# Performance work log

Hardware: AMD Instinct MI355X
Metric: run time of the kernel (lower is better)

Reference implementation:

```python
import jax, jax.numpy as jnp
import numpy as np

N_NODES = 100000
N_EDGES = 3200000  # avg degree 32
IN_FEATS = 512
N_HIDDEN = 128
N_CLASSES = 64
K = 10  # n_layers of gated APPNP propagation


def setup_inputs() -> dict:
    key = jax.random.key(0)
    ks = jax.random.split(key, 6)
    features = jax.random.normal(ks[0], (N_NODES, IN_FEATS), dtype=jnp.float32)
    W1 = jax.random.normal(ks[1], (IN_FEATS, N_HIDDEN), dtype=jnp.float32) * (1.0 / np.sqrt(IN_FEATS))
    b1 = jnp.zeros((N_HIDDEN,), jnp.float32)
    W2 = jax.random.normal(ks[2], (N_HIDDEN, N_CLASSES), dtype=jnp.float32) * (1.0 / np.sqrt(N_HIDDEN))
    b2 = jnp.zeros((N_CLASSES,), jnp.float32)
    init_weight_y = jax.random.normal(ks[3], (IN_FEATS, N_CLASSES), dtype=jnp.float32) * (1.0 / np.sqrt(IN_FEATS))
    edge_index = jax.random.randint(ks[4], (2, N_EDGES), 0, N_NODES, dtype=jnp.int32)
    return {
        "features": features, "W1": W1, "b1": b1, "W2": W2, "b2": b2,
        "init_weight_y": init_weight_y, "edge_index": edge_index,
    }


def reference(features, W1, b1, W2, b2, init_weight_y, edge_index):
    # Eval-mode forward: feat/edge dropout are identity.
    src, dst = edge_index[0], edge_index[1]
    n = features.shape[0]
    # Symmetric GCN normalization D^{-1/2} A D^{-1/2} from in-degrees.
    deg = jax.ops.segment_sum(jnp.ones(src.shape, features.dtype), dst, num_segments=n)
    norm = jax.lax.rsqrt(jnp.clip(deg, 1.0))
    ew = (norm[src] * norm[dst])[:, None]  # [E,1] edge weights

    def spmm(x):  # A_hat @ x via gather-multiply-scatter
        return jax.ops.segment_sum(x[src] * ew, dst, num_segments=n)

    # feature transform: dropout(identity) -> linear -> relu
    h = jax.nn.relu(features @ W1 + b1)                      # [N,H]
    logits = jax.nn.softmax(features @ init_weight_y, axis=1)  # [N,C]
    # project predictions before propagation (APPNP propagates class scores)
    h0 = h @ W2 + b2                                         # [N,C]

    def step(carry, _):
        hc, lg = carry
        agg_lg = spmm(lg)                                    # neighbor soft labels
        # gate: per-node agreement between own and aggregated soft labels
        z = jax.nn.sigmoid(jnp.sum(lg * agg_lg, axis=1, keepdims=True))  # [N,1]
        h_new = z * spmm(hc) + (1.0 - z) * h0                # gated APPNP hop
        return (h_new, agg_lg), None

    (h_out, _), _ = jax.lax.scan(step, (h0, logits), None, length=K)
    return h_out
```

## Files before the change

kernel.cpp:

```cpp
#include <hip/hip_runtime.h>

typedef __attribute__((ext_vector_type(8))) short bf16x8;
typedef __attribute__((ext_vector_type(4))) short bf16x4;
typedef __attribute__((ext_vector_type(4))) float f32x4;
typedef __attribute__((ext_vector_type(4))) unsigned int u32x4;

__device__ __forceinline__ unsigned short f2bf(float f) {
  unsigned int u = __float_as_uint(f);
  u += 0x7fffu + ((u >> 16) & 1u);
  return (unsigned short)(u >> 16);
}
__device__ __forceinline__ float bflo(unsigned int w) { return __uint_as_float(w << 16); }
__device__ __forceinline__ float bfhi(unsigned int w) { return __uint_as_float(w & 0xffff0000u); }

__device__ __forceinline__ short* ldsp(short* base, int row, int rowbytes, int colshort) {
  int off = row * rowbytes + colshort * 2;
  off ^= ((row & 7) << 4);
  return (short*)((char*)base + off);
}

#define CHUNK 8192
#define NBMAX 512

__global__ __launch_bounds__(256) void k_bhist(const int* __restrict__ ei, int E, int NB,
                                               int* __restrict__ gcnt, int* __restrict__ wghist) {
  __shared__ int h[NBMAX];
  for (int t = threadIdx.x; t < NB; t += 256) h[t] = 0;
  __syncthreads();
  int base = blockIdx.x * CHUNK;
#pragma unroll
  for (int i = 0; i < CHUNK / 256; ++i) {
    int e = base + i * 256 + threadIdx.x;
    if (e < E) atomicAdd(&h[ei[E + e] >> 8], 1);
  }
  __syncthreads();
  for (int t = threadIdx.x; t < NB; t += 256) {
    int c = h[t];
    wghist[blockIdx.x * NBMAX + t] = c;
    if (c) atomicAdd(&gcnt[t], c);
  }
}

__global__ void k_bscan(const int* __restrict__ gcnt, int* __restrict__ bbase,
                        int* __restrict__ gcur, int* __restrict__ offs, int NB, int N) {
  __shared__ int sm[512];
  int t = threadIdx.x;
  int v = (t < NB) ? gcnt[t] : 0;
  sm[t] = v;
  __syncthreads();
  for (int o = 1; o < 512; o <<= 1) {
    int x = (t >= o) ? sm[t - o] : 0;
    __syncthreads();
    sm[t] += x;
    __syncthreads();
  }
  if (t < NB) { int e = sm[t] - v; bbase[t] = e; gcur[t] = e; }
  if (t == 511) { bbase[NB] = sm[511]; offs[N] = sm[511]; }
}

__global__ __launch_bounds__(256) void k_bucket(const int* __restrict__ ei,
                                                const int* __restrict__ wghist,
                                                int* __restrict__ gcur,
                                                int2* __restrict__ bpairs, int E, int NB) {
  __shared__ int lbase[NBMAX];
  __shared__ int lcur[NBMAX];
  for (int t = threadIdx.x; t < NB; t += 256) {
    int c = wghist[blockIdx.x * NBMAX + t];
    lbase[t] = c ? atomicAdd(&gcur[t], c) : 0;
    lcur[t] = 0;
  }
  __syncthreads();
  int base = blockIdx.x * CHUNK;
#pragma unroll
  for (int i = 0; i < CHUNK / 256; ++i) {
    int e = base + i * 256 + threadIdx.x;
    if (e < E) {
      int s = ei[e], d = ei[E + e];
      int b = d >> 8;
      int p = lbase[b] + atomicAdd(&lcur[b], 1);
      bpairs[p] = make_int2(s, d);
    }
  }
}

__global__ __launch_bounds__(256) void k_csr(const int2* __restrict__ bpairs,
                                             const int* __restrict__ bbase,
                                             int* __restrict__ offs, float* __restrict__ nrm,
                                             int* __restrict__ csr_src, int N) {
  __shared__ int hist[256];
  __shared__ int scan[256];
  __shared__ int cur[256];
  const int t = threadIdx.x;
  const int b = blockIdx.x;
  const int d0 = b << 8;
  const int nn = min(256, N - d0);
  const int base = bbase[b], end = bbase[b + 1];
  hist[t] = 0;
  __syncthreads();
  for (int e = base + t; e < end; e += 256) atomicAdd(&hist[bpairs[e].y - d0], 1);
  __syncthreads();
  int myc = hist[t];
  scan[t] = myc;
  __syncthreads();
  for (int o = 1; o < 256; o <<= 1) {
    int x = (t >= o) ? scan[t - o] : 0;
    __syncthreads();
    scan[t] += x;
    __syncthreads();
  }
  int excl = scan[t] - myc;
  if (t < nn) {
    offs[d0 + t] = base + excl;
    nrm[d0 + t] = rsqrtf(fmaxf((float)myc, 1.f));
  }
  cur[t] = excl;
  __syncthreads();
  for (int e = base + t; e < end; e += 256) {
    int2 pr = bpairs[e];
    int pos = atomicAdd(&cur[pr.y - d0], 1);
    csr_src[base + pos] = pr.x;
  }
}

__global__ void k_wprep(const float* __restrict__ W1, const float* __restrict__ Wy,
                        unsigned short* __restrict__ Wt) {
  int k = blockIdx.x, j = threadIdx.x;
  float v = (j < 128) ? W1[k * 128 + j] : Wy[k * 64 + (j - 128)];
  Wt[j * 512 + k] = f2bf(v);
}
__global__ void k_wprep2(const float* __restrict__ W2, unsigned short* __restrict__ Wt2) {
  int k = blockIdx.x, j = threadIdx.x;
  Wt2[j * 128 + k] = f2bf(W2[k * 64 + j]);
}

__global__ __launch_bounds__(256) void k_transform(
    const unsigned short* __restrict__ Wt, const unsigned short* __restrict__ Wt2,
    const float* __restrict__ X, const float* __restrict__ b1, const float* __restrict__ b2,
    const float* __restrict__ nrm,
    unsigned int* __restrict__ pk0, unsigned short* __restrict__ h0b, int n)
{
  __shared__ short Xs[128 * 32];
  __shared__ short Ws[192 * 32];
  __shared__ short Hs[128 * 128];
  __shared__ short W2s[64 * 128];

  const int tid = threadIdx.x;
  const int w = tid >> 6;
  const int lane = tid & 63;
  const int c = lane & 15;
  const int g = lane >> 4;
  const int m0 = blockIdx.x * 128;

#pragma unroll
  for (int i = 0; i < 4; ++i) {
    int cc = tid + i * 256;
    int j2 = cc >> 4, k8 = (cc & 15) * 8;
    bf16x8 v = *(const bf16x8*)&Wt2[j2 * 128 + k8];
    *(bf16x8*)ldsp(W2s, j2, 256, k8) = v;
  }

  f32x4 zero4 = {0.f, 0.f, 0.f, 0.f};
  f32x4 acc[2][12];
#pragma unroll
  for (int mi = 0; mi < 2; ++mi)
#pragma unroll
    for (int i = 0; i < 12; ++i) acc[mi][i] = zero4;

  const int xr = tid >> 1;
  const int xc = (tid & 1) * 16;
  const int xrow = m0 + xr;

  for (int kk = 0; kk < 512; kk += 32) {
    float4 f[4];
    if (xrow < n) {
      const float4* p = (const float4*)(X + (size_t)xrow * 512 + kk + xc);
      f[0] = p[0]; f[1] = p[1]; f[2] = p[2]; f[3] = p[3];
    } else {
      float4 z = {0.f, 0.f, 0.f, 0.f};
      f[0] = z; f[1] = z; f[2] = z; f[3] = z;
    }
    bf16x8 lo, hi;
    {
      const float* fp = (const float*)f;
#pragma unroll
      for (int q = 0; q < 8; ++q) { lo[q] = (short)f2bf(fp[q]); hi[q] = (short)f2bf(fp[8 + q]); }
    }
    *(bf16x8*)ldsp(Xs, xr, 64, xc) = lo;
    *(bf16x8*)ldsp(Xs, xr, 64, xc + 8) = hi;
#pragma unroll
    for (int i = 0; i < 3; ++i) {
      int cc = tid + i * 256;
      int j = cc >> 2, k8 = (cc & 3) * 8;
      bf16x8 v = *(const bf16x8*)&Wt[j * 512 + kk + k8];
      *(bf16x8*)ldsp(Ws, j, 64, k8) = v;
    }
    __syncthreads();
    bf16x8 bx0 = *(const bf16x8*)ldsp(Xs, w * 32 + c, 64, g * 8);
    bf16x8 bx1 = *(const bf16x8*)ldsp(Xs, w * 32 + 16 + c, 64, g * 8);
#pragma unroll
    for (int jt = 0; jt < 12; ++jt) {
      bf16x8 aw = *(const bf16x8*)ldsp(Ws, jt * 16 + c, 64, g * 8);
      acc[0][jt] = __builtin_amdgcn_mfma_f32_16x16x32_bf16(aw, bx0, acc[0][jt], 0, 0, 0);
      acc[1][jt] = __builtin_amdgcn_mfma_f32_16x16x32_bf16(aw, bx1, acc[1][jt], 0, 0, 0);
    }
    __syncthreads();
  }

  float lv[2][16];
  float inv_[2];
#pragma unroll
  for (int mi = 0; mi < 2; ++mi) {
    int m = w * 32 + mi * 16 + c;
#pragma unroll
    for (int jt = 0; jt < 8; ++jt) {
      int jb = jt * 16 + g * 4;
      bf16x4 hv;
#pragma unroll
      for (int q = 0; q < 4; ++q) {
        float hvf = fmaxf(acc[mi][jt][q] + b1[jb + q], 0.f);
        hv[q] = (short)f2bf(hvf);
      }
      *(bf16x4*)ldsp(Hs, m, 256, jb) = hv;
    }
    float mx = -3.4e38f;
#pragma unroll
    for (int t = 0; t < 4; ++t)
#pragma unroll
      for (int q = 0; q < 4; ++q) {
        float vv = acc[mi][8 + t][q];
        lv[mi][t * 4 + q] = vv;
        mx = fmaxf(mx, vv);
      }
    mx = fmaxf(mx, __shfl_xor(mx, 16, 64));
    mx = fmaxf(mx, __shfl_xor(mx, 32, 64));
    float sum = 0.f;
#pragma unroll
    for (int i = 0; i < 16; ++i) { lv[mi][i] = __expf(lv[mi][i] - mx); sum += lv[mi][i]; }
    sum += __shfl_xor(sum, 16, 64);
    sum += __shfl_xor(sum, 32, 64);
    inv_[mi] = 1.f / sum;
  }
  __syncthreads();

  f32x4 acc2[2][4];
#pragma unroll
  for (int mi = 0; mi < 2; ++mi)
#pragma unroll
    for (int i = 0; i < 4; ++i) acc2[mi][i] = zero4;
#pragma unroll
  for (int kk2 = 0; kk2 < 4; ++kk2) {
    bf16x8 bh0 = *(const bf16x8*)ldsp(Hs, w * 32 + c, 256, kk2 * 32 + g * 8);
    bf16x8 bh1 = *(const bf16x8*)ldsp(Hs, w * 32 + 16 + c, 256, kk2 * 32 + g * 8);
#pragma unroll
    for (int j2t = 0; j2t < 4; ++j2t) {
      bf16x8 a2 = *(const bf16x8*)ldsp(W2s, j2t * 16 + c, 256, kk2 * 32 + g * 8);
      acc2[0][j2t] = __builtin_amdgcn_mfma_f32_16x16x32_bf16(a2, bh0, acc2[0][j2t], 0, 0, 0);
      acc2[1][j2t] = __builtin_amdgcn_mfma_f32_16x16x32_bf16(a2, bh1, acc2[1][j2t], 0, 0, 0);
    }
  }

#pragma unroll
  for (int mi = 0; mi < 2; ++mi) {
    int m = w * 32 + mi * 16 + c;
    int grow = m0 + m;
    if (grow < n) {
      float nd = nrm[grow];
#pragma unroll
      for (int t = 0; t < 4; ++t) {
        int cb = t * 16 + g * 4;
        u32x4 pkv;
        bf16x4 hb;
#pragma unroll
        for (int q = 0; q < 4; ++q) {
          float lg  = lv[mi][t * 4 + q] * inv_[mi];
          float h0v = acc2[mi][t][q] + b2[cb + q];
          hb[q]  = (short)f2bf(h0v);
          pkv[q] = ((unsigned)f2bf(nd * h0v) << 16) | (unsigned)f2bf(nd * lg);
        }
        *(u32x4*)(pk0 + (size_t)grow * 64 + cb) = pkv;
        *(bf16x4*)(h0b + (size_t)grow * 64 + cb) = hb;
      }
    }
  }
}

__global__ __launch_bounds__(256) void k_prop(
    const int* __restrict__ offs, const int* __restrict__ csr_src,
    const unsigned int* __restrict__ pk_in, unsigned int* __restrict__ pk_out,
    const unsigned short* __restrict__ h0b, const float* __restrict__ nrm,
    float* __restrict__ final_out, int n, int last)
{
  const int lane = threadIdx.x & 63;
  const int node = blockIdx.x * 4 + (threadIdx.x >> 6);
  if (node >= n) return;
  const int beg = offs[node], end = offs[node + 1];

  float aL0 = 0.f, aL1 = 0.f, aH0 = 0.f, aH1 = 0.f;
  int e = beg;
  for (; e + 8 <= end; e += 8) {
    int s0 = csr_src[e + 0], s1 = csr_src[e + 1], s2 = csr_src[e + 2], s3 = csr_src[e + 3];
    int s4 = csr_src[e + 4], s5 = csr_src[e + 5], s6 = csr_src[e + 6], s7 = csr_src[e + 7];
    unsigned w0 = pk_in[(size_t)s0 * 64 + lane];
    unsigned w1 = pk_in[(size_t)s1 * 64 + lane];
    unsigned w2 = pk_in[(size_t)s2 * 64 + lane];
    unsigned w3 = pk_in[(size_t)s3 * 64 + lane];
    unsigned w4 = pk_in[(size_t)s4 * 64 + lane];
    unsigned w5 = pk_in[(size_t)s5 * 64 + lane];
    unsigned w6 = pk_in[(size_t)s6 * 64 + lane];
    unsigned w7 = pk_in[(size_t)s7 * 64 + lane];
    aL0 += bflo(w0) + bflo(w1) + bflo(w2) + bflo(w3);
    aL1 += bflo(w4) + bflo(w5) + bflo(w6) + bflo(w7);
    aH0 += bfhi(w0) + bfhi(w1) + bfhi(w2) + bfhi(w3);
    aH1 += bfhi(w4) + bfhi(w5) + bfhi(w6) + bfhi(w7);
  }
  for (; e < end; ++e) {
    unsigned w = pk_in[(size_t)csr_src[e] * 64 + lane];
    aL0 += bflo(w);
    aH0 += bfhi(w);
  }
  float aL = aL0 + aL1;
  float aH = aH0 + aH1;

  size_t base = (size_t)node * 64 + lane;
  float p = bflo(pk_in[base]) * aL;
#pragma unroll
  for (int off = 32; off >= 1; off >>= 1) p += __shfl_xor(p, off, 64);
  float z = 1.f / (1.f + __expf(-p));

  float nd = nrm[node];
  float h0v = __uint_as_float((unsigned)h0b[base] << 16);
  float hn = z * nd * aH + (1.f - z) * h0v;

  if (last) {
    final_out[base] = hn;
  } else {
    pk_out[base] = ((unsigned)f2bf(nd * hn) << 16) | (unsigned)f2bf(nd * nd * aL);
  }
}

extern "C" void kernel_launch(void* const* d_in, const int* in_sizes, int n_in,
                              void* d_out, int out_size, void* d_ws, size_t ws_size,
                              hipStream_t stream) {
  (void)n_in; (void)out_size; (void)ws_size;
  const float* X  = (const float*)d_in[0];
  const float* W1 = (const float*)d_in[1];
  const float* b1 = (const float*)d_in[2];
  const float* W2 = (const float*)d_in[3];
  const float* b2 = (const float*)d_in[4];
  const float* Wy = (const float*)d_in[5];
  const int*   ei = (const int*)d_in[6];
  const int N = in_sizes[0] / 512;
  const int E = in_sizes[6] / 2;
  const int NB = (N + 255) >> 8;
  const int NWG = (E + CHUNK - 1) / CHUNK;

  char* p = (char*)d_ws;
  auto alloc = [&](size_t bytes) -> char* {
    char* r = p; p += (bytes + 255) & ~(size_t)255; return r;
  };
  int*            gcnt    = (int*)  alloc(NBMAX * 4);
  int*            bbase   = (int*)  alloc((NBMAX + 1) * 4);
  int*            gcur    = (int*)  alloc(NBMAX * 4);
  int*            wghist  = (int*)  alloc((size_t)NWG * NBMAX * 4);
  int*            offs    = (int*)  alloc((size_t)(N + 1) * 4);
  float*          nrm     = (float*)alloc((size_t)N * 4);
  int*            csr_src = (int*)  alloc((size_t)E * 4);
  unsigned short* Wt      = (unsigned short*)alloc(192 * 512 * 2);
  unsigned short* Wt2     = (unsigned short*)alloc(64 * 128 * 2);
  size_t pkbytes = (size_t)N * 64 * 4;
  size_t bpbytes = (size_t)E * 8;
  char*           shared0 = alloc(pkbytes > bpbytes ? pkbytes : bpbytes);
  int2*           bpairs  = (int2*)shared0;
  unsigned int*   pkA     = (unsigned int*)shared0;
  unsigned int*   pkB     = (unsigned int*)alloc(pkbytes);
  unsigned short* h0b     = (unsigned short*)alloc((size_t)N * 64 * 2);

  hipMemsetAsync(gcnt, 0, NBMAX * 4, stream);

  k_wprep<<<512, 192, 0, stream>>>(W1, Wy, Wt);
  k_wprep2<<<128, 64, 0, stream>>>(W2, Wt2);
  k_bhist<<<NWG, 256, 0, stream>>>(ei, E, NB, gcnt, wghist);
  k_bscan<<<1, 512, 0, stream>>>(gcnt, bbase, gcur, offs, NB, N);
  k_bucket<<<NWG, 256, 0, stream>>>(ei, wghist, gcur, bpairs, E, NB);
  k_csr<<<NB, 256, 0, stream>>>(bpairs, bbase, offs, nrm, csr_src, N);
  k_transform<<<(N + 127) / 128, 256, 0, stream>>>(Wt, Wt2, X, b1, b2, nrm, pkA, h0b, N);

  for (int k = 0; k < 10; ++k) {
    const unsigned int* in  = (k & 1) ? pkB : pkA;
    unsigned int*       out = (k & 1) ? pkA : pkB;
    k_prop<<<(N + 3) / 4, 256, 0, stream>>>(offs, csr_src, in, out, h0b, nrm,
                                            (float*)d_out, N, (k == 9) ? 1 : 0);
  }
}
```

Before: 1.341 ms.

## Convert CSR to padded 4-node ELL groups with 16-byte vector gathers in propagation

Builds a padded ELL-style index array in which each group of 4 destination nodes is padded to its largest degree. Indices are pre-shifted to byte offsets, and padding points to a zero row appended to the packed feature buffers. k_prop now gives each wave 4 nodes, with 16 lanes per node loading 16-byte vectors, so fewer lanes are spent per edge and the gathers get wider. The cost is extra preprocessing (a three-kernel scan plus ELL construction), more index memory, and wasted loads on padded slots when degrees within a group are uneven.

```diff
diff --git a/kernel.cpp b/kernel.cpp
--- a/kernel.cpp
+++ b/kernel.cpp
@@ -86,7 +86,8 @@
 __global__ __launch_bounds__(256) void k_csr(const int2* __restrict__ bpairs,
                                              const int* __restrict__ bbase,
                                              int* __restrict__ offs, float* __restrict__ nrm,
-                                             int* __restrict__ csr_src, int N) {
+                                             int* __restrict__ csr_src,
+                                             int* __restrict__ gslots, int N) {
   __shared__ int hist[256];
   __shared__ int scan[256];
   __shared__ int cur[256];
@@ -113,12 +114,83 @@
     offs[d0 + t] = base + excl;
     nrm[d0 + t] = rsqrtf(fmaxf((float)myc, 1.f));
   }
+  if (t < 64) {
+    int w0 = hist[4 * t + 0], w1 = hist[4 * t + 1];
+    int w2 = hist[4 * t + 2], w3 = hist[4 * t + 3];
+    gslots[b * 64 + t] = 4 * max(max(w0, w1), max(w2, w3));
+  }
   cur[t] = excl;
   __syncthreads();
   for (int e = base + t; e < end; e += 256) {
     int2 pr = bpairs[e];
     int pos = atomicAdd(&cur[pr.y - d0], 1);
     csr_src[base + pos] = pr.x;
+  }
+}
+
+__global__ void k_scan1(const int* __restrict__ in, int* __restrict__ out,
+                        int* __restrict__ bsum, int n) {
+  __shared__ int sm[1024];
+  int t = threadIdx.x;
+  int gid = blockIdx.x * 1024 + t;
+  int v = (gid < n) ? in[gid] : 0;
+  sm[t] = v;
+  __syncthreads();
+  for (int off = 1; off < 1024; off <<= 1) {
+    int x = (t >= off) ? sm[t - off] : 0;
+    __syncthreads();
+    sm[t] += x;
+    __syncthreads();
+  }
+  if (gid < n) out[gid] = sm[t] - v;
+  if (t == 1023) bsum[blockIdx.x] = sm[1023];
+}
+
+__global__ void k_scan2(int* __restrict__ bsum, int nb) {
+  __shared__ int sm[128];
+  int t = threadIdx.x;
+  int v = (t < nb) ? bsum[t] : 0;
+  sm[t] = v;
+  __syncthreads();
+  for (int o = 1; o < 128; o <<= 1) {
+    int x = (t >= o) ? sm[t - o] : 0;
+    __syncthreads();
+    sm[t] += x;
+    __syncthreads();
+  }
+  if (t < nb) bsum[t] = sm[t] - v;
+  if (t == 127) bsum[nb] = sm[127];
+}
+
+__global__ void k_scan3(int* __restrict__ out, const int* __restrict__ bsum, int n) {
+  int gid = blockIdx.x * 1024 + threadIdx.x;
+  if (gid < n) out[gid] += bsum[blockIdx.x];
+  if (gid == 0) out[n] = bsum[gridDim.x];
+}
+
+__global__ __launch_bounds__(64) void k_ell(
+    const int* __restrict__ offs, const int* __restrict__ csr_src,
+    const int* __restrict__ gof, unsigned* __restrict__ pidx,
+    unsigned int* __restrict__ pkA, unsigned int* __restrict__ pkB, int N) {
+  int g = blockIdx.x;
+  int t = threadIdx.x;
+  if (g == 0) {
+    pkA[(size_t)N * 64 + t] = 0;
+    pkB[(size_t)N * 64 + t] = 0;
+  }
+  int base = gof[g];
+  int slots = gof[g + 1] - base;
+  int o[4], d[4];
+#pragma unroll
+  for (int s = 0; s < 4; ++s) {
+    int nd_ = g * 4 + s;
+    o[s] = (nd_ < N) ? offs[nd_] : 0;
+    d[s] = (nd_ < N) ? (offs[nd_ + 1] - o[s]) : 0;
+  }
+  unsigned zoff = (unsigned)N << 8;
+  for (int j = t; j < slots; j += 64) {
+    int i = j >> 2, s = j & 3;
+    pidx[base + j] = (i < d[s]) ? ((unsigned)csr_src[o[s] + i] << 8) : zoff;
   }
 }
 
@@ -285,56 +357,78 @@
 }
 
 __global__ __launch_bounds__(256) void k_prop(
-    const int* __restrict__ offs, const int* __restrict__ csr_src,
+    const int* __restrict__ gof, const unsigned* __restrict__ pidx,
     const unsigned int* __restrict__ pk_in, unsigned int* __restrict__ pk_out,
     const unsigned short* __restrict__ h0b, const float* __restrict__ nrm,
-    float* __restrict__ final_out, int n, int last)
+    float* __restrict__ final_out, int n, int ng, int last)
 {
   const int lane = threadIdx.x & 63;
-  const int node = blockIdx.x * 4 + (threadIdx.x >> 6);
+  const int g = blockIdx.x * 4 + (threadIdx.x >> 6);
+  if (g >= ng) return;
+  const int sub = lane >> 4;
+  const int cq  = lane & 15;
+  const int node = g * 4 + sub;
+  const int beg = gof[g];
+  const int w = (gof[g + 1] - beg) >> 2;
+  const char* pkc = (const char*)pk_in;
+  const unsigned* ib = pidx + beg + sub;
+  const int coff = cq << 4;
+
+  float aL[4] = {0.f, 0.f, 0.f, 0.f}, aH[4] = {0.f, 0.f, 0.f, 0.f};
+  float bL[4] = {0.f, 0.f, 0.f, 0.f}, bH[4] = {0.f, 0.f, 0.f, 0.f};
+  int i = 0;
+  for (; i + 2 <= w; i += 2) {
+    unsigned r0 = ib[4 * i];
+    unsigned r1 = ib[4 * i + 4];
+    u32x4 w0 = *(const u32x4*)(pkc + r0 + coff);
+    u32x4 w1 = *(const u32x4*)(pkc + r1 + coff);
+#pragma unroll
+    for (int q = 0; q < 4; ++q) {
+      aL[q] += bflo(w0[q]); aH[q] += bfhi(w0[q]);
+      bL[q] += bflo(w1[q]); bH[q] += bfhi(w1[q]);
+    }
+  }
+  if (i < w) {
+    unsigned r0 = ib[4 * i];
+    u32x4 w0 = *(const u32x4*)(pkc + r0 + coff);
+#pragma unroll
+    for (int q = 0; q < 4; ++q) { aL[q] += bflo(w0[q]); aH[q] += bfhi(w0[q]); }
+  }
+#pragma unroll
+  for (int q = 0; q < 4; ++q) { aL[q] += bL[q]; aH[q] += bH[q]; }
+
   if (node >= n) return;
-  const int beg = offs[node], end = offs[node + 1];
-
-  float aL0 = 0.f, aL1 = 0.f, aH0 = 0.f, aH1 = 0.f;
-  int e = beg;
-  for (; e + 8 <= end; e += 8) {
-    int s0 = csr_src[e + 0], s1 = csr_src[e + 1], s2 = csr_src[e + 2], s3 = csr_src[e + 3];
-    int s4 = csr_src[e + 4], s5 = csr_src[e + 5], s6 = csr_src[e + 6], s7 = csr_src[e + 7];
-    unsigned w0 = pk_in[(size_t)s0 * 64 + lane];
-    unsigned w1 = pk_in[(size_t)s1 * 64 + lane];
-    unsigned w2 = pk_in[(size_t)s2 * 64 + lane];
-    unsigned w3 = pk_in[(size_t)s3 * 64 + lane];
-    unsigned w4 = pk_in[(size_t)s4 * 64 + lane];
-    unsigned w5 = pk_in[(size_t)s5 * 64 + lane];
-    unsigned w6 = pk_in[(size_t)s6 * 64 + lane];
-    unsigned w7 = pk_in[(size_t)s7 * 64 + lane];
-    aL0 += bflo(w0) + bflo(w1) + bflo(w2) + bflo(w3);
-    aL1 += bflo(w4) + bflo(w5) + bflo(w6) + bflo(w7);
-    aH0 += bfhi(w0) + bfhi(w1) + bfhi(w2) + bfhi(w3);
-    aH1 += bfhi(w4) + bfhi(w5) + bfhi(w6) + bfhi(w7);
-  }
-  for (; e < end; ++e) {
-    unsigned w = pk_in[(size_t)csr_src[e] * 64 + lane];
-    aL0 += bflo(w);
-    aH0 += bfhi(w);
-  }
-  float aL = aL0 + aL1;
-  float aH = aH0 + aH1;
-
-  size_t base = (size_t)node * 64 + lane;
-  float p = bflo(pk_in[base]) * aL;
-#pragma unroll
-  for (int off = 32; off >= 1; off >>= 1) p += __shfl_xor(p, off, 64);
+  u32x4 own = *(const u32x4*)(pkc + (node << 8) + coff);
+  float p = 0.f;
+#pragma unroll
+  for (int q = 0; q < 4; ++q) p += bflo(own[q]) * aL[q];
+  p += __shfl_xor(p, 1, 64);
+  p += __shfl_xor(p, 2, 64);
+  p += __shfl_xor(p, 4, 64);
+  p += __shfl_xor(p, 8, 64);
   float z = 1.f / (1.f + __expf(-p));
-
   float nd = nrm[node];
-  float h0v = __uint_as_float((unsigned)h0b[base] << 16);
-  float hn = z * nd * aH + (1.f - z) * h0v;
+  bf16x4 h0v = *(const bf16x4*)(h0b + (size_t)node * 64 + cq * 4);
 
   if (last) {
-    final_out[base] = hn;
+    float4 o;
+    float* op = &o.x;
+#pragma unroll
+    for (int q = 0; q < 4; ++q) {
+      float h0f = __uint_as_float(((unsigned)(unsigned short)h0v[q]) << 16);
+      op[q] = z * nd * aH[q] + (1.f - z) * h0f;
+    }
+    *(float4*)(final_out + (size_t)node * 64 + cq * 4) = o;
   } else {
-    pk_out[base] = ((unsigned)f2bf(nd * hn) << 16) | (unsigned)f2bf(nd * nd * aL);
+    u32x4 pkv;
+    float nn2 = nd * nd;
+#pragma unroll
+    for (int q = 0; q < 4; ++q) {
+      float h0f = __uint_as_float(((unsigned)(unsigned short)h0v[q]) << 16);
+      float hn = z * nd * aH[q] + (1.f - z) * h0f;
+      pkv[q] = ((unsigned)f2bf(nd * hn) << 16) | (unsigned)f2bf(nn2 * aL[q]);
+    }
+    *(u32x4*)((char*)pk_out + (node << 8) + coff) = pkv;
   }
 }
 
@@ -352,6 +446,7 @@
   const int N = in_sizes[0] / 512;
   const int E = in_sizes[6] / 2;
   const int NB = (N + 255) >> 8;
+  const int NG = NB * 64;
   const int NWG = (E + CHUNK - 1) / CHUNK;
 
   char* p = (char*)d_ws;
@@ -365,9 +460,13 @@
   int*            offs    = (int*)  alloc((size_t)(N + 1) * 4);
   float*          nrm     = (float*)alloc((size_t)N * 4);
   int*            csr_src = (int*)  alloc((size_t)E * 4);
+  int*            gslots  = (int*)  alloc((size_t)(NG + 1) * 4);
+  int*            gof     = (int*)  alloc((size_t)(NG + 1) * 4);
+  int*            sbsum   = (int*)  alloc(1024);
+  unsigned*       pidx    = (unsigned*)alloc((size_t)2 * E * 4);
   unsigned short* Wt      = (unsigned short*)alloc(192 * 512 * 2);
   unsigned short* Wt2     = (unsigned short*)alloc(64 * 128 * 2);
-  size_t pkbytes = (size_t)N * 64 * 4;
+  size_t pkbytes = (size_t)(N + 1) * 64 * 4;
   size_t bpbytes = (size_t)E * 8;
   char*           shared0 = alloc(pkbytes > bpbytes ? pkbytes : bpbytes);
   int2*           bpairs  = (int2*)shared0;
@@ -382,13 +481,18 @@
   k_bhist<<<NWG, 256, 0, stream>>>(ei, E, NB, gcnt, wghist);
   k_bscan<<<1, 512, 0, stream>>>(gcnt, bbase, gcur, offs, NB, N);
   k_bucket<<<NWG, 256, 0, stream>>>(ei, wghist, gcur, bpairs, E, NB);
-  k_csr<<<NB, 256, 0, stream>>>(bpairs, bbase, offs, nrm, csr_src, N);
+  k_csr<<<NB, 256, 0, stream>>>(bpairs, bbase, offs, nrm, csr_src, gslots, N);
+  int nb2 = (NG + 1023) / 1024;
+  k_scan1<<<nb2, 1024, 0, stream>>>(gslots, gof, sbsum, NG);
+  k_scan2<<<1, 128, 0, stream>>>(sbsum, nb2);
+  k_scan3<<<nb2, 1024, 0, stream>>>(gof, sbsum, NG);
+  k_ell<<<NG, 64, 0, stream>>>(offs, csr_src, gof, pidx, pkA, pkB, N);
   k_transform<<<(N + 127) / 128, 256, 0, stream>>>(Wt, Wt2, X, b1, b2, nrm, pkA, h0b, N);
 
   for (int k = 0; k < 10; ++k) {
     const unsigned int* in  = (k & 1) ? pkB : pkA;
     unsigned int*       out = (k & 1) ? pkA : pkB;
-    k_prop<<<(N + 3) / 4, 256, 0, stream>>>(offs, csr_src, in, out, h0b, nrm,
-                                            (float*)d_out, N, (k == 9) ? 1 : 0);
-  }
-}
+    k_prop<<<(NG + 3) / 4, 256, 0, stream>>>(gof, pidx, in, out, h0b, nrm,
+                                             (float*)d_out, N, NG, (k == 9) ? 1 : 0);
+  }
+}
```

After: 1.334 ms. Within noise of the previous version (-0.5%).
